# Optimization experiments

Measured on AMD Instinct MI355X. Metric: run time of the kernel, lower is better.

The kernel has to match this reference:

```python
import math
import jax, jax.numpy as jnp
import numpy as np

N_HEAD = 16
ROPE_BASE = 10000.0


def _qk_norm(x, scale):
    # RMSNorm over head_dim, eps added inside sqrt as in the torch code
    norm = jnp.sqrt(jnp.mean(x.astype(jnp.float32) ** 2, axis=-1, keepdims=True) + 1e-6)
    return (x.astype(jnp.float32) / norm * scale).astype(x.dtype)


def _rope3d(q, k, coords, token_type):
    # q,k: [B,H,T,D]; coords: [B,T,3]; token_type: [B,T]
    # head_dim is split into 3 equal chunks, chunk i rotated by coords[...,i].
    # Tokens with token_type == 0 (e.g. text tokens) are left unrotated.
    B, H, T, D = q.shape
    d3 = D // 3
    half = d3 // 2
    inv_freq = ROPE_BASE ** (-jnp.arange(half, dtype=jnp.float32) / half)  # [half]

    def rotate(x):
        # x: [B,H,T,D] -> rotate each of the 3 axis-chunks
        chunks = []
        for a in range(3):
            xa = x[..., a * d3:(a + 1) * d3]                       # [B,H,T,d3]
            ang = coords[:, None, :, a, None] * inv_freq            # [B,1,T,half]
            cos, sin = jnp.cos(ang), jnp.sin(ang)
            x1, x2 = xa[..., :half], xa[..., half:]
            chunks.append(jnp.concatenate([x1 * cos - x2 * sin,
                                           x1 * sin + x2 * cos], axis=-1))
        rot = jnp.concatenate(chunks, axis=-1)
        apply = (token_type > 0)[:, None, :, None]                  # [B,1,T,1]
        return jnp.where(apply, rot, x)

    return rotate(q), rotate(k)


def setup_inputs() -> dict:
    key = jax.random.key(0)
    ks = jax.random.split(key, 5)
    B, T, C = 2, 2048, 1536
    D = C // N_HEAD
    return {
        "x": jax.random.normal(ks[0], (B, T, C), jnp.float32),
        "coords": jax.random.uniform(ks[1], (B, T, 3), jnp.float32) * 32.0,
        "token_type": jax.random.randint(ks[2], (B, T), 0, 2),
        "W_qkv": jax.random.normal(ks[3], (3 * C, C), jnp.float32) * (1.0 / math.sqrt(C)),
        "W_out": jax.random.normal(ks[4], (C, C), jnp.float32) * (1.0 / math.sqrt(C)),
        "q_scale": jnp.ones((D,), jnp.float32),
        "k_scale": jnp.ones((D,), jnp.float32),
    }


def reference(x, coords, token_type, W_qkv, W_out, q_scale, k_scale):
    B, T, C = x.shape
    H = N_HEAD
    D = C // H
    qkv = x @ W_qkv.T                                   # [B,T,3C]
    q, k, v = jnp.split(qkv, 3, axis=-1)
    q = q.reshape(B, T, H, D).transpose(0, 2, 1, 3)     # [B,H,T,D]
    k = k.reshape(B, T, H, D).transpose(0, 2, 1, 3)
    v = v.reshape(B, T, H, D).transpose(0, 2, 1, 3)
    q = _qk_norm(q, q_scale)
    k = _qk_norm(k, k_scale)
    q, k = _rope3d(q, k, coords, token_type)
    scale = 1.0 / math.sqrt(D)
    attn = jnp.einsum('bhqd,bhkd->bhqk', q, k) * scale  # [B,H,T,T]
    causal = jnp.tril(jnp.ones((T, T), bool))
    attn = jnp.where(causal, attn, -jnp.inf)
    attn = jax.nn.softmax(attn, axis=-1)
    out = jnp.einsum('bhqk,bhkd->bhqd', attn, v)        # [B,H,T,D]
    out = out.transpose(0, 2, 1, 3).reshape(B, T, C)
    return out @ W_out.T
```

## Files before the change

### kernel.cpp

```cpp
#include <hip/hip_runtime.h>
#include <stdint.h>
#include <stddef.h>


typedef __attribute__((ext_vector_type(8))) __bf16 bf16x8;
typedef __attribute__((ext_vector_type(4))) __bf16 bf16x4;
typedef __attribute__((ext_vector_type(4))) float  f32x4;

#define NB 2
#define NT 2048
#define NC 1536
#define NH 16
#define ND 96
#define NQKV 4608
#define NM 4096

static __device__ __forceinline__ float fexp2(float x) {
#if __has_builtin(__builtin_amdgcn_exp2f)
  return __builtin_amdgcn_exp2f(x);
#else
  return exp2f(x);
#endif
}

static __device__ __forceinline__ void g2lds16(const void* g, void* l) {
  __builtin_amdgcn_global_load_lds(
      (const __attribute__((address_space(1))) void*)g,
      (__attribute__((address_space(3))) void*)l, 16, 0, 0);
}

__global__ __launch_bounds__(256) void cvt3_f32_bf16(
    const float4* __restrict__ sx, bf16x4* __restrict__ dx, int n4x,
    const float4* __restrict__ sw, bf16x4* __restrict__ dw, int n4w,
    const float4* __restrict__ so, bf16x4* __restrict__ do_) {
  int i = blockIdx.x * 256 + threadIdx.x;
  const float4* s;
  bf16x4* d;
  if (i < n4x)            { s = sx + i;               d = dx + i; }
  else if (i < n4x + n4w) { s = sw + (i - n4x);       d = dw + (i - n4x); }
  else                    { s = so + (i - n4x - n4w); d = do_ + (i - n4x - n4w); }
  float4 v = *s;
  bf16x4 o;
  o[0] = (__bf16)v.x; o[1] = (__bf16)v.y;
  o[2] = (__bf16)v.z; o[3] = (__bf16)v.w;
  *d = o;
}

#define BAR1() do { __builtin_amdgcn_s_barrier(); \
                    asm volatile("" ::: "memory"); } while (0)
#define BAR2() do { asm volatile("" ::: "memory"); \
                    __builtin_amdgcn_s_barrier(); } while (0)
#define WAITLGKM() do { asm volatile("s_waitcnt lgkmcnt(0)" ::: "memory"); \
                        __builtin_amdgcn_sched_barrier(0); } while (0)
#define WAITVM6() asm volatile("s_waitcnt vmcnt(6)" ::: "memory")
#define WAITVM5() asm volatile("s_waitcnt vmcnt(5)" ::: "memory")

template <int MH>
static __device__ __forceinline__ void readA2(
    bf16x8 (&aR)[2][2], const char* buf, int aro, int sk0, int sk1) {
#pragma unroll
  for (int i = 0; i < 2; ++i) {
    const char* p = buf + aro + (MH * 2 + i) * 2048;
    aR[i][0] = *(const bf16x8*)(p + sk0);
    aR[i][1] = *(const bf16x8*)(p + sk1);
  }
}
template <int NF0, int NN>
static __device__ __forceinline__ void readBN(
    bf16x8 (&bb)[NN][2], const char* buf, int bro, int sk0, int sk1) {
#pragma unroll
  for (int j = 0; j < NN; ++j) {
    const char* p = buf + bro + (NF0 + j) * 2048;
    bb[j][0] = *(const bf16x8*)(p + sk0);
    bb[j][1] = *(const bf16x8*)(p + sk1);
  }
}
template <int MH, int NF0, int NN>
static __device__ __forceinline__ void quadN(
    f32x4 (&acc)[4][9], const bf16x8 (&aR)[2][2], const bf16x8 (&bb)[NN][2]) {
  __builtin_amdgcn_s_setprio(1);
#pragma unroll
  for (int i = 0; i < 2; ++i)
#pragma unroll
    for (int j = 0; j < NN; ++j)
#pragma unroll
      for (int ks = 0; ks < 2; ++ks)
        acc[MH * 2 + i][NF0 + j] = __builtin_amdgcn_mfma_f32_16x16x32_bf16(
            aR[i][ks], bb[j][ks], acc[MH * 2 + i][NF0 + j], 0, 0, 0);
  __builtin_amdgcn_s_setprio(0);
}

__global__ __launch_bounds__(512, 2) void gemm1_8ph(
    const __bf16* __restrict__ A, const __bf16* __restrict__ Bw,
    __bf16* __restrict__ C, int M, int N, int K) {
  __shared__ __align__(16) char lds[139264];
  char* const A0 = lds;
  char* const A1 = lds + 32768;
  char* const B0 = lds + 65536;
  char* const B1 = lds + 102400;

  const int tid = threadIdx.x;
  const int l   = tid & 63;
  const int w   = tid >> 6;
  const int wm  = w >> 1;
  const int wn  = w & 1;
  const int lm  = l & 15;
  const int lq  = l >> 4;

  const int nnt = 16;
  const int nwg = gridDim.x * gridDim.y;
  const int lid = blockIdx.y * gridDim.x + blockIdx.x;
  const int swz = (lid & 7) * (nwg >> 3) + (lid >> 3);
  const int m0  = (swz / nnt) * 256;
  const int n0  = (swz % nnt) * 288;

  const int aro = (wm * 64 + lm) * 128;
  const int bro = (wn * 144 + lm) * 128;
  const int sk0 = ((lq) ^ (lm & 7)) * 16;
  const int sk1 = ((4 + lq) ^ (lm & 7)) * 16;

  const int ssl = ((l & 7) ^ ((l >> 3) & 7)) * 8;
  auto stageA = [&](int grow0, int k0, char* dst) {
#pragma unroll
    for (int q2 = 0; q2 < 2; ++q2) {
      const int c   = w * 2 + q2;
      const int row = c * 8 + (l >> 3);
      g2lds16(A + (size_t)(grow0 + row) * K + k0 + ssl, dst + c * 1024);
    }
  };
  auto stageB = [&](int grow0, int k0, char* dst) {
#pragma unroll
    for (int q2 = 0; q2 < 2; ++q2) {
      const int c   = w * 2 + q2;
      const int row = c * 8 + (l >> 3);
      g2lds16(Bw + (size_t)(grow0 + row) * K + k0 + ssl, dst + c * 1024);
    }
    if (w < 2) {
      const int c   = 16 + w;
      const int row = c * 8 + (l >> 3);
      g2lds16(Bw + (size_t)(grow0 + row) * K + k0 + ssl, dst + c * 1024);
    }
  };

  f32x4 acc[4][9] = {};
  bf16x8 aL[2][2], aH[2][2], b5[5][2], b4[4][2];

  stageA(m0,       0,  A0);
  stageA(m0 + 128, 0,  A0 + 16384);
  stageB(n0,       0,  B0);
  stageB(n0 + 144, 0,  B0 + 18432);
  stageA(m0,       64, A1);
  stageA(m0 + 128, 64, A1 + 16384);

  const int NIT = K >> 7;
  for (int it = 0; it < NIT; ++it) {
    const int kh  = it * 128 + 64;
    const int knl = it * 128 + 128;
    const int knh = it * 128 + 192;
    stageB(n0, kh, B1);
    WAITVM6();
    BAR1();
    readA2<0>(aL, A0, aro, sk0, sk1);
    readBN<0, 5>(b5, B0, bro, sk0, sk1);
    WAITLGKM();
    quadN<0, 0, 5>(acc, aL, b5);
    BAR2();
    stageB(n0 + 144, kh, B1 + 18432);
    BAR1();
    readA2<1>(aH, A0, aro, sk0, sk1);
    WAITLGKM();
    quadN<1, 0, 5>(acc, aH, b5);
    BAR2();
    stageA(m0, knl, A0);
    BAR1();
    readBN<5, 4>(b4, B0, bro, sk0, sk1);
    WAITLGKM();
    quadN<1, 5, 4>(acc, aH, b4);
    BAR2();
    stageA(m0 + 128, knl, A0 + 16384);
    BAR1();
    quadN<0, 5, 4>(acc, aL, b4);
    BAR2();
    stageB(n0, knl, B0);
    WAITVM6();
    BAR1();
    readA2<0>(aL, A1, aro, sk0, sk1);
    readBN<0, 5>(b5, B1, bro, sk0, sk1);
    WAITLGKM();
    quadN<0, 0, 5>(acc, aL, b5);
    BAR2();
    stageB(n0 + 144, knl, B0 + 18432);
    BAR1();
    readA2<1>(aH, A1, aro, sk0, sk1);
    WAITLGKM();
    quadN<1, 0, 5>(acc, aH, b5);
    BAR2();
    stageA(m0, knh, A1);
    BAR1();
    readBN<5, 4>(b4, B1, bro, sk0, sk1);
    WAITLGKM();
    quadN<1, 5, 4>(acc, aH, b4);
    BAR2();
    stageA(m0 + 128, knh, A1 + 16384);
    BAR1();
    quadN<0, 5, 4>(acc, aL, b4);
    BAR2();
  }

  const int r0 = lq * 4;
#pragma unroll
  for (int mf = 0; mf < 4; ++mf)
#pragma unroll
    for (int nf = 0; nf < 9; ++nf)
#pragma unroll
      for (int r = 0; r < 4; ++r) {
        const size_t row = (size_t)(m0 + wm * 64 + mf * 16 + r0 + r);
        const size_t col = (size_t)(n0 + wn * 144 + nf * 16 + lm);
        C[row * N + col] = (__bf16)acc[mf][nf][r];
      }
}

template <int MH, int NF0, int NN>
static __device__ __forceinline__ void g2quad(
    f32x4 (&acc)[4][3], const bf16x8 (&aR)[2][2], const bf16x8 (&bb)[NN][2]) {
  __builtin_amdgcn_s_setprio(1);
#pragma unroll
  for (int i = 0; i < 2; ++i)
#pragma unroll
    for (int j = 0; j < NN; ++j)
#pragma unroll
      for (int ks = 0; ks < 2; ++ks)
        acc[MH * 2 + i][NF0 + j] = __builtin_amdgcn_mfma_f32_16x16x32_bf16(
            aR[i][ks], bb[j][ks], acc[MH * 2 + i][NF0 + j], 0, 0, 0);
  __builtin_amdgcn_s_setprio(0);
}

__global__ __launch_bounds__(512, 2) void gemm2_8ph(
    const __bf16* __restrict__ A, const __bf16* __restrict__ Bw,
    float* __restrict__ C, int M, int N, int K) {
  __shared__ __align__(16) char lds[81920];
  char* const A0 = lds;
  char* const A1 = lds + 16384;
  char* const B0 = lds + 32768;
  char* const B1 = lds + 57344;

  const int tid = threadIdx.x;
  const int l   = tid & 63;
  const int w   = tid >> 6;
  const int wm  = w >> 2;
  const int wn  = w & 3;
  const int lm  = l & 15;
  const int lq  = l >> 4;

  const int nwg = gridDim.x * gridDim.y;
  const int lid = blockIdx.y * gridDim.x + blockIdx.x;
  const int swz = (lid & 7) * (nwg >> 3) + (lid >> 3);
  const int m0  = (swz / 8) * 128;
  const int n0  = (swz % 8) * 192;

  const int aro = (wm * 64 + lm) * 128;
  const int bro = (wn * 48 + lm) * 128;
  const int sk0 = ((lq) ^ (lm & 7)) * 16;
  const int sk1 = ((4 + lq) ^ (lm & 7)) * 16;

  const int ssl = ((l & 7) ^ ((l >> 3) & 7)) * 8;
  auto stageA = [&](int k0, char* dst) {
#pragma unroll
    for (int q2 = 0; q2 < 2; ++q2) {
      const int c   = w * 2 + q2;
      const int row = c * 8 + (l >> 3);
      g2lds16(A + (size_t)(m0 + row) * K + k0 + ssl, dst + c * 1024);
    }
  };
  auto stageB = [&](int k0, char* dst) {
#pragma unroll
    for (int q2 = 0; q2 < 3; ++q2) {
      const int c   = w * 3 + q2;
      const int row = c * 8 + (l >> 3);
      g2lds16(Bw + (size_t)(n0 + row) * K + k0 + ssl, dst + c * 1024);
    }
  };

  f32x4 acc[4][3] = {};
  bf16x8 aL[2][2], aH[2][2], bL[2][2], bH[1][2];

  stageA(0,  A0);
  stageB(0,  B0);
  stageA(64, A1);

  const int NIT = K >> 7;
  for (int it = 0; it < NIT; ++it) {
    const int kh  = it * 128 + 64;
    const int knl = it * 128 + 128;
    const int knh = it * 128 + 192;
    stageB(kh, B1);
    WAITVM5();
    BAR1();
    readA2<0>(aL, A0, aro, sk0, sk1);
    readBN<0, 2>(bL, B0, bro, sk0, sk1);
    WAITLGKM();
    g2quad<0, 0, 2>(acc, aL, bL);
    BAR2();
    BAR1();
    readA2<1>(aH, A0, aro, sk0, sk1);
    WAITLGKM();
    g2quad<1, 0, 2>(acc, aH, bL);
    BAR2();
    stageA(knl, A0);
    BAR1();
    readBN<2, 1>(bH, B0, bro, sk0, sk1);
    WAITLGKM();
    g2quad<1, 2, 1>(acc, aH, bH);
    BAR2();
    BAR1();
    g2quad<0, 2, 1>(acc, aL, bH);
    BAR2();
    stageB(knl, B0);
    WAITVM5();
    BAR1();
    readA2<0>(aL, A1, aro, sk0, sk1);
    readBN<0, 2>(bL, B1, bro, sk0, sk1);
    WAITLGKM();
    g2quad<0, 0, 2>(acc, aL, bL);
    BAR2();
    BAR1();
    readA2<1>(aH, A1, aro, sk0, sk1);
    WAITLGKM();
    g2quad<1, 0, 2>(acc, aH, bL);
    BAR2();
    stageA(knh, A1);
    BAR1();
    readBN<2, 1>(bH, B1, bro, sk0, sk1);
    WAITLGKM();
    g2quad<1, 2, 1>(acc, aH, bH);
    BAR2();
    BAR1();
    g2quad<0, 2, 1>(acc, aL, bH);
    BAR2();
  }

  const int r0 = lq * 4;
#pragma unroll
  for (int mf = 0; mf < 4; ++mf)
#pragma unroll
    for (int nf = 0; nf < 3; ++nf)
#pragma unroll
      for (int r = 0; r < 4; ++r) {
        const size_t row = (size_t)(m0 + wm * 64 + mf * 16 + r0 + r);
        const size_t col = (size_t)(n0 + wn * 48 + nf * 16 + lm);
        C[row * N + col] = acc[mf][nf][r];
      }
}

static __device__ __forceinline__ float rope_one(float v, float p, int d,
                                                 const float* c3) {
  const int a  = d >> 5;
  const int j  = d & 31;
  const int jj = j & 15;
  const float invf = fexp2((float)jj * -0.8304820237218406f);
  const float ang  = c3[a] * invf;
  float sn, cs;
  __sincosf(ang, &sn, &cs);
  return (j < 16) ? (v * cs - p * sn) : (v * cs + p * sn);
}

__global__ __launch_bounds__(256) void normrope_kernel(
    const __bf16* __restrict__ qkv, const float* __restrict__ coords,
    const int* __restrict__ ttype, const float* __restrict__ qsc,
    const float* __restrict__ ksc, __bf16* __restrict__ qo,
    __bf16* __restrict__ ko) {
  const int l   = threadIdx.x & 63;
  const int w   = threadIdx.x >> 6;
  const int rid = blockIdx.x * 4 + w;
  const int h   = rid & (NH - 1);
  const int bt  = rid >> 4;
  const int t   = bt & (NT - 1);
  const int b   = bt >> 11;
  const __bf16* base = qkv + (size_t)bt * NQKV + h * ND;
  const float*  c3   = coords + (size_t)bt * 3;
  const bool rope    = ttype[bt] > 0;
  const size_t bh    = (size_t)(b * NH + h);

  {
    float x0 = (float)base[l];
    float x1 = (l < 32) ? (float)base[64 + l] : 0.f;
    float ss = x0 * x0 + x1 * x1;
#pragma unroll
    for (int off = 1; off < 64; off <<= 1) ss += __shfl_xor(ss, off, 64);
    const float rn = rsqrtf(ss * (1.f / 96.f) + 1e-6f);
    x0 *= rn * qsc[l];
    if (l < 32) x1 *= rn * qsc[64 + l];
    const float p0 = __shfl_xor(x0, 16, 64);
    const float p1 = __shfl_xor(x1, 16, 64);
    if (rope) {
      x0 = rope_one(x0, p0, l, c3);
      if (l < 32) x1 = rope_one(x1, p1, 64 + l, c3);
    }
    __bf16* dst = qo + (bh * NT + t) * ND;
    dst[l] = (__bf16)x0;
    if (l < 32) dst[64 + l] = (__bf16)x1;
  }
  {
    float x0 = (float)base[NC + l];
    float x1 = (l < 32) ? (float)base[NC + 64 + l] : 0.f;
    float ss = x0 * x0 + x1 * x1;
#pragma unroll
    for (int off = 1; off < 64; off <<= 1) ss += __shfl_xor(ss, off, 64);
    const float rn = rsqrtf(ss * (1.f / 96.f) + 1e-6f);
    x0 *= rn * ksc[l];
    if (l < 32) x1 *= rn * ksc[64 + l];
    const float p0 = __shfl_xor(x0, 16, 64);
    const float p1 = __shfl_xor(x1, 16, 64);
    if (rope) {
      x0 = rope_one(x0, p0, l, c3);
      if (l < 32) x1 = rope_one(x1, p1, 64 + l, c3);
    }
    __bf16* dst = ko + (bh * NT + t) * ND;
    dst[l] = (__bf16)x0;
    if (l < 32) dst[64 + l] = (__bf16)x1;
  }
}

__global__ __launch_bounds__(256) void transpose_v(
    const __bf16* __restrict__ qkv, __bf16* __restrict__ vo) {
  __shared__ __align__(16) __bf16 tile[96][264];
  const int tid = threadIdx.x;
  const int bh  = blockIdx.y;
  const int t0  = blockIdx.x * 256;
  const int b   = bh >> 4, h = bh & 15;
  const __bf16* src =
      qkv + ((size_t)(b * NT + t0 + tid)) * NQKV + 2 * NC + h * ND;
#pragma unroll
  for (int ch = 0; ch < 12; ++ch) {
    bf16x8 v = *(const bf16x8*)(src + ch * 8);
#pragma unroll
    for (int j = 0; j < 8; ++j) tile[ch * 8 + j][tid] = v[j];
  }
  __syncthreads();
#pragma unroll
  for (int k = 0; k < 12; ++k) {
    const int c  = tid + k * 256;
    const int d  = c >> 5;
    const int tc = c & 31;
    bf16x8 v = *(const bf16x8*)(&tile[d][tc * 8]);
    *(bf16x8*)(vo + ((size_t)bh * ND + d) * NT + t0 + tc * 8) = v;
  }
}

static __device__ __forceinline__ void attn_tile64(
    const bf16x8 (&aq)[3], const bf16x8 (&bk)[4][3], int q0r, int n0,
    int lm, int lq, f32x4& lsum, __bf16* pbase ) {
  f32x4 s[4];
#pragma unroll
  for (int nt = 0; nt < 4; ++nt) {
    f32x4 a = {};
#pragma unroll
    for (int c = 0; c < 3; ++c)
      a = __builtin_amdgcn_mfma_f32_16x16x32_bf16(aq[c], bk[nt][c], a, 0, 0, 0);
    s[nt] = a;
  }
  if (n0 + 63 > q0r) {
#pragma unroll
    for (int nt = 0; nt < 4; ++nt)
#pragma unroll
      for (int r = 0; r < 4; ++r)
        if (n0 + nt * 16 + lm > q0r + lq * 4 + r) s[nt][r] = -1e30f;
  }
  const float cl = 0.10206207261596575f * 1.4426950408889634f;
#pragma unroll
  for (int nt = 0; nt < 4; ++nt)
#pragma unroll
    for (int r = 0; r < 4; ++r)
      s[nt][r] = fexp2((s[nt][r] - 96.0f) * cl);
#pragma unroll
  for (int r = 0; r < 4; ++r)
    lsum[r] += (s[0][r] + s[1][r]) + (s[2][r] + s[3][r]);
#pragma unroll
  for (int nt = 0; nt < 4; ++nt)
#pragma unroll
    for (int r = 0; r < 4; ++r)
      pbase[(nt >> 1) * 640 + (lq * 4 + r) * 40 + (nt & 1) * 16 + lm] =
          (__bf16)s[nt][r];
}

__global__ __launch_bounds__(512) void attn_fwd2(
    const __bf16* __restrict__ q, const __bf16* __restrict__ k,
    const __bf16* __restrict__ vt, __bf16* __restrict__ out) {
  __shared__ __align__(16) char KV[2][24576];
  __shared__ __align__(16) __bf16 plds[8][2][2][16][40];
  const int tid = threadIdx.x;
  const int l   = tid & 63;
  const int w   = tid >> 6;

  const int i_  = blockIdx.y * 8 + blockIdx.x;
  const int slot = i_ >> 3;
  const int bh  = (i_ & 7) + 8 * (slot & 3);
  const int qp  = slot >> 2;

  const int lm  = l & 15;
  const int lq  = l >> 4;
  const int q0L = qp * 128 + w * 16;
  const int q0H = (15 - qp) * 128 + w * 16;
  const int nktLw = qp * 2 + (w >> 2) + 1;
  const int nktHw = (15 - qp) * 2 + (w >> 2) + 1;
  const int nkt   = (15 - qp) * 2 + 2;
  const __bf16* qh = q  + (size_t)bh * NT * ND;
  const __bf16* kh = k  + (size_t)bh * NT * ND;
  const __bf16* vh = vt + (size_t)bh * ND * NT;
  __bf16* pbL = &plds[w][0][0][0][0];
  __bf16* pbH = &plds[w][1][0][0][0];

  auto stage = [&](int n0, char* buf) {
#pragma unroll
    for (int q2 = 0; q2 < 3; ++q2) {
      const int g = w * 3 + q2;
      if (g < 12) {
        const int nt = g / 3, c = g - nt * 3;
        g2lds16(kh + (size_t)(n0 + nt * 16 + (l >> 2)) * ND + c * 32 + (l & 3) * 8,
                buf + g * 1024);
      } else {
        const int gv = g - 12;
        const int dt = gv >> 1, hf = gv & 1;
        g2lds16(vh + (size_t)(dt * 16 + (l >> 2)) * NT + n0 + hf * 32 + (l & 3) * 8,
                buf + 12288 + gv * 1024);
      }
    }
  };

  bf16x8 aqL[3], aqH[3];
#pragma unroll
  for (int c = 0; c < 3; ++c) {
    aqL[c] = *(const bf16x8*)(qh + (size_t)(q0L + lm) * ND + c * 32 + lq * 8);
    aqH[c] = *(const bf16x8*)(qh + (size_t)(q0H + lm) * ND + c * 32 + lq * 8);
  }

  f32x4 oL[6] = {}, oH[6] = {};
  f32x4 lsL = {}, lsH = {};
  const int ji = (lm * 4 + lq) * 16;

  stage(0, KV[0]);
  for (int kt = 0; kt < nkt; ++kt) {
    __syncthreads();
    if (kt + 1 < nkt) stage((kt + 1) * 64, KV[(kt + 1) & 1]);
    const char* Kc = KV[kt & 1];
    const char* Vc = KV[kt & 1] + 12288;
    const int n0 = kt * 64;
    bf16x8 bk[4][3];
#pragma unroll
    for (int nt = 0; nt < 4; ++nt)
#pragma unroll
      for (int c = 0; c < 3; ++c)
        bk[nt][c] = *(const bf16x8*)(Kc + (nt * 3 + c) * 1024 + ji);
    const bool doL = kt < nktLw;
    const bool doH = kt < nktHw;
    if (doL) attn_tile64(aqL, bk, q0L, n0, lm, lq, lsL, pbL);
    if (doH) attn_tile64(aqH, bk, q0H, n0, lm, lq, lsH, pbH);
    bf16x8 apL0 = {}, apL1 = {}, apH0 = {}, apH1 = {};
    if (doL) {
      apL0 = *(const bf16x8*)(pbL + lm * 40 + lq * 8);
      apL1 = *(const bf16x8*)(pbL + 640 + lm * 40 + lq * 8);
    }
    if (doH) {
      apH0 = *(const bf16x8*)(pbH + lm * 40 + lq * 8);
      apH1 = *(const bf16x8*)(pbH + 640 + lm * 40 + lq * 8);
    }
#pragma unroll
    for (int dt = 0; dt < 6; ++dt) {
      bf16x8 bv0 = *(const bf16x8*)(Vc + (dt * 2 + 0) * 1024 + ji);
      bf16x8 bv1 = *(const bf16x8*)(Vc + (dt * 2 + 1) * 1024 + ji);
      if (doL) {
        oL[dt] = __builtin_amdgcn_mfma_f32_16x16x32_bf16(apL0, bv0, oL[dt], 0, 0, 0);
        oL[dt] = __builtin_amdgcn_mfma_f32_16x16x32_bf16(apL1, bv1, oL[dt], 0, 0, 0);
      }
      if (doH) {
        oH[dt] = __builtin_amdgcn_mfma_f32_16x16x32_bf16(apH0, bv0, oH[dt], 0, 0, 0);
        oH[dt] = __builtin_amdgcn_mfma_f32_16x16x32_bf16(apH1, bv1, oH[dt], 0, 0, 0);
      }
    }
  }

  const int b = bh >> 4, h = bh & 15;
#pragma unroll
  for (int f = 0; f < 2; ++f) {
    const f32x4* o = f ? oH : oL;
    const f32x4& ls = f ? lsH : lsL;
    const int q0 = f ? q0H : q0L;
    float rl[4];
#pragma unroll
    for (int r = 0; r < 4; ++r) {
      float v = ls[r];
#pragma unroll
      for (int off = 1; off < 16; off <<= 1) v += __shfl_xor(v, off, 64);
      rl[r] = 1.f / v;
    }
#pragma unroll
    for (int dt = 0; dt < 6; ++dt)
#pragma unroll
      for (int r = 0; r < 4; ++r) {
        const int t = q0 + lq * 4 + r;
        out[((size_t)(b * NT + t)) * NC + h * ND + dt * 16 + lm] =
            (__bf16)(o[dt][r] * rl[r]);
      }
  }
}

static constexpr size_t OFF_XB   = 0;
static constexpr size_t OFF_WQKV = 12582912;
static constexpr size_t OFF_WOUT = 26738688;
static constexpr size_t OFF_QKV  = 31457280;
static constexpr size_t OFF_Q    = 69206016;
static constexpr size_t OFF_K    = 81788928;
static constexpr size_t OFF_VT   = 94371840;

extern "C" void kernel_launch(void* const* d_in, const int* in_sizes, int n_in,
                              void* d_out, int out_size, void* d_ws,
                              size_t ws_size, hipStream_t stream) {
  const float* x      = (const float*)d_in[0];
  const float* coords = (const float*)d_in[1];
  const int*   ttype  = (const int*)d_in[2];
  const float* wqkv   = (const float*)d_in[3];
  const float* wout   = (const float*)d_in[4];
  const float* qs     = (const float*)d_in[5];
  const float* ks     = (const float*)d_in[6];

  char* ws = (char*)d_ws;
  __bf16* xb    = (__bf16*)(ws + OFF_XB);
  __bf16* wqkvb = (__bf16*)(ws + OFF_WQKV);
  __bf16* woutb = (__bf16*)(ws + OFF_WOUT);
  __bf16* qkvb  = (__bf16*)(ws + OFF_QKV);
  __bf16* qb    = (__bf16*)(ws + OFF_Q);
  __bf16* kb    = (__bf16*)(ws + OFF_K);
  __bf16* vtb   = (__bf16*)(ws + OFF_VT);
  __bf16* attnb = (__bf16*)(ws + OFF_XB);

  {
    const int n4x = NM * NC / 4;
    const int n4w = NQKV * NC / 4;
    const int n4o = NC * NC / 4;
    const int nblk = (n4x + n4w + n4o) / 256;
    cvt3_f32_bf16<<<nblk, 256, 0, stream>>>(
        (const float4*)x, (bf16x4*)xb, n4x,
        (const float4*)wqkv, (bf16x4*)wqkvb, n4w,
        (const float4*)wout, (bf16x4*)woutb);
  }
  gemm1_8ph<<<dim3(NQKV / 288, NM / 256), 512, 0, stream>>>(
      xb, wqkvb, qkvb, NM, NQKV, NC);
  normrope_kernel<<<(NB * NT * NH) / 4, 256, 0, stream>>>(
      qkvb, coords, ttype, qs, ks, qb, kb);
  transpose_v<<<dim3(NT / 256, NB * NH), 256, 0, stream>>>(qkvb, vtb);
  attn_fwd2<<<dim3(8, NB * NH), 512, 0, stream>>>(qb, kb, vtb, attnb);
  gemm2_8ph<<<dim3(NC / 192, NM / 128), 512, 0, stream>>>(
      attnb, woutb, (float*)d_out, NM, NC, NC);
}
```

Baseline: 286.7 us.

## Fuse QK RMSNorm, 3D RoPE and V transpose into QKV GEMM epilogue

The QKV projection GEMM now stages its output tile in LDS and applies the per-head RMSNorm and 3D RoPE to Q and K, and transposes V, writing the attention-ready layouts directly. This removes the separate normrope and transpose kernels, two launches, and the write and re-read of the full bf16 QKV intermediate. In exchange the GEMM epilogue becomes serial and heavier, because each head row is handled by a single thread and some threads sit idle. The launch bound no longer requests two blocks per CU, which may lower occupancy.

```diff
diff --git a/kernel.cpp b/kernel.cpp
--- a/kernel.cpp
+++ b/kernel.cpp
@@ -90,9 +90,12 @@
   __builtin_amdgcn_s_setprio(0);
 }
 
-__global__ __launch_bounds__(512, 2) void gemm1_8ph(
+__global__ __launch_bounds__(512) void gemm1_8ph(
     const __bf16* __restrict__ A, const __bf16* __restrict__ Bw,
-    __bf16* __restrict__ C, int M, int N, int K) {
+    const float* __restrict__ coords, const int* __restrict__ ttype,
+    const float* __restrict__ qsc, const float* __restrict__ ksc,
+    __bf16* __restrict__ qo, __bf16* __restrict__ ko,
+    __bf16* __restrict__ vo, int M, int N, int K) {
   __shared__ __align__(16) char lds[139264];
   char* const A0 = lds;
   char* const A1 = lds + 32768;
@@ -207,17 +210,124 @@
     BAR2();
   }
 
-  const int r0 = lq * 4;
-#pragma unroll
-  for (int mf = 0; mf < 4; ++mf)
-#pragma unroll
-    for (int nf = 0; nf < 9; ++nf)
-#pragma unroll
-      for (int r = 0; r < 4; ++r) {
-        const size_t row = (size_t)(m0 + wm * 64 + mf * 16 + r0 + r);
-        const size_t col = (size_t)(n0 + wn * 144 + nf * 16 + lm);
-        C[row * N + col] = (__bf16)acc[mf][nf][r];
+  asm volatile("s_waitcnt vmcnt(0)" ::: "memory");
+  __syncthreads();
+  constexpr int S = 296;
+  __bf16* cl = (__bf16*)lds;
+  const int bI = m0 >> 11;
+  const float IF[16] = {
+      1.0f, 0.5623413251903491f, 0.31622776601683794f, 0.17782794100389226f,
+      0.1f, 0.05623413251903491f, 0.03162277660168379f,
+      0.017782794100389229f, 0.01f, 0.005623413251903491f,
+      0.0031622776601683794f, 0.0017782794100389228f, 0.001f,
+      0.0005623413251903491f, 0.00031622776601683794f,
+      0.00017782794100389227f};
+  for (int half = 0; half < 2; ++half) {
+    if ((wm >> 1) == half) {
+#pragma unroll
+      for (int mf = 0; mf < 4; ++mf)
+#pragma unroll
+        for (int nf = 0; nf < 9; ++nf)
+#pragma unroll
+          for (int r = 0; r < 4; ++r)
+            cl[((wm & 1) * 64 + mf * 16 + lq * 4 + r) * S + wn * 144 +
+               nf * 16 + lm] = (__bf16)acc[mf][nf][r];
+    }
+    __syncthreads();
+    const int rbase = m0 + half * 128;
+    const int tb    = rbase & 2047;
+    const int nact  = half ? 512 : 256;
+    if (tid < nact) {
+      for (int tk = tid; tk < 384; tk += nact) {
+        const int j    = tk >> 7;
+        const int rowl = tk & 127;
+        const int g    = n0 / 96 + j;
+        const int ty   = g >> 4;
+        if (ty < 2) {
+          const int hh   = g & 15;
+          const int rowg = rbase + rowl;
+          const float* c3 = coords + (size_t)rowg * 3;
+          const bool rp   = ttype[rowg] > 0;
+          const float* sc = ty ? ksc : qsc;
+          const __bf16* lr = cl + rowl * S + j * 96;
+          float ss = 0.f;
+#pragma unroll
+          for (int c8 = 0; c8 < 12; ++c8) {
+            bf16x8 v = *(const bf16x8*)(lr + c8 * 8);
+#pragma unroll
+            for (int e = 0; e < 8; ++e) {
+              const float f = (float)v[e];
+              ss += f * f;
+            }
+          }
+          const float rn = rsqrtf(ss * (1.f / 96.f) + 1e-6f);
+          __bf16* dst = (ty ? ko : qo) +
+              ((size_t)((bI * 16 + hh) * 2048 + (rowg & 2047))) * 96;
+#pragma unroll
+          for (int a = 0; a < 3; ++a) {
+            const float ca = c3[a];
+            float xl[16], xh[16];
+            bf16x8 v0 = *(const bf16x8*)(lr + a * 32);
+            bf16x8 v1 = *(const bf16x8*)(lr + a * 32 + 8);
+            bf16x8 v2 = *(const bf16x8*)(lr + a * 32 + 16);
+            bf16x8 v3 = *(const bf16x8*)(lr + a * 32 + 24);
+#pragma unroll
+            for (int e = 0; e < 8; ++e) {
+              xl[e]     = (float)v0[e] * rn * sc[a * 32 + e];
+              xl[e + 8] = (float)v1[e] * rn * sc[a * 32 + 8 + e];
+              xh[e]     = (float)v2[e] * rn * sc[a * 32 + 16 + e];
+              xh[e + 8] = (float)v3[e] * rn * sc[a * 32 + 24 + e];
+            }
+            if (rp) {
+#pragma unroll
+              for (int e = 0; e < 16; ++e) {
+                float sn, csn;
+                __sincosf(ca * IF[e], &sn, &csn);
+                const float lo = xl[e] * csn - xh[e] * sn;
+                const float hi = xl[e] * sn + xh[e] * csn;
+                xl[e] = lo;
+                xh[e] = hi;
+              }
+            }
+            bf16x8 o0, o1, o2, o3;
+#pragma unroll
+            for (int e = 0; e < 8; ++e) {
+              o0[e] = (__bf16)xl[e];
+              o1[e] = (__bf16)xl[e + 8];
+              o2[e] = (__bf16)xh[e];
+              o3[e] = (__bf16)xh[e + 8];
+            }
+            *(bf16x8*)(dst + a * 32)      = o0;
+            *(bf16x8*)(dst + a * 32 + 8)  = o1;
+            *(bf16x8*)(dst + a * 32 + 16) = o2;
+            *(bf16x8*)(dst + a * 32 + 24) = o3;
+          }
+        }
       }
+#pragma unroll
+      for (int j = 0; j < 3; ++j) {
+        const int g = n0 / 96 + j;
+        if (g >= 32) {
+          const int hh = g & 15;
+          for (int tk = tid; tk < 192; tk += nact) {
+            const int d  = tk >> 1;
+            const int sg = tk & 1;
+            const __bf16* cp = cl + (sg * 64) * S + j * 96 + d;
+            __bf16* vdst = vo +
+                ((size_t)(bI * 16 + hh) * 96 + d) * 2048 + tb + sg * 64;
+#pragma unroll
+            for (int vv = 0; vv < 8; ++vv) {
+              bf16x8 ov;
+#pragma unroll
+              for (int e = 0; e < 8; ++e) ov[e] = cp[(vv * 8 + e) * S];
+              *(bf16x8*)(vdst + vv * 8) = ov;
+            }
+          }
+        }
+      }
+    }
+    __syncthreads();
+  }
 }
 
 template <int MH, int NF0, int NN>
@@ -350,101 +460,6 @@
         const size_t col = (size_t)(n0 + wn * 48 + nf * 16 + lm);
         C[row * N + col] = acc[mf][nf][r];
       }
-}
-
-static __device__ __forceinline__ float rope_one(float v, float p, int d,
-                                                 const float* c3) {
-  const int a  = d >> 5;
-  const int j  = d & 31;
-  const int jj = j & 15;
-  const float invf = fexp2((float)jj * -0.8304820237218406f);
-  const float ang  = c3[a] * invf;
-  float sn, cs;
-  __sincosf(ang, &sn, &cs);
-  return (j < 16) ? (v * cs - p * sn) : (v * cs + p * sn);
-}
-
-__global__ __launch_bounds__(256) void normrope_kernel(
-    const __bf16* __restrict__ qkv, const float* __restrict__ coords,
-    const int* __restrict__ ttype, const float* __restrict__ qsc,
-    const float* __restrict__ ksc, __bf16* __restrict__ qo,
-    __bf16* __restrict__ ko) {
-  const int l   = threadIdx.x & 63;
-  const int w   = threadIdx.x >> 6;
-  const int rid = blockIdx.x * 4 + w;
-  const int h   = rid & (NH - 1);
-  const int bt  = rid >> 4;
-  const int t   = bt & (NT - 1);
-  const int b   = bt >> 11;
-  const __bf16* base = qkv + (size_t)bt * NQKV + h * ND;
-  const float*  c3   = coords + (size_t)bt * 3;
-  const bool rope    = ttype[bt] > 0;
-  const size_t bh    = (size_t)(b * NH + h);
-
-  {
-    float x0 = (float)base[l];
-    float x1 = (l < 32) ? (float)base[64 + l] : 0.f;
-    float ss = x0 * x0 + x1 * x1;
-#pragma unroll
-    for (int off = 1; off < 64; off <<= 1) ss += __shfl_xor(ss, off, 64);
-    const float rn = rsqrtf(ss * (1.f / 96.f) + 1e-6f);
-    x0 *= rn * qsc[l];
-    if (l < 32) x1 *= rn * qsc[64 + l];
-    const float p0 = __shfl_xor(x0, 16, 64);
-    const float p1 = __shfl_xor(x1, 16, 64);
-    if (rope) {
-      x0 = rope_one(x0, p0, l, c3);
-      if (l < 32) x1 = rope_one(x1, p1, 64 + l, c3);
-    }
-    __bf16* dst = qo + (bh * NT + t) * ND;
-    dst[l] = (__bf16)x0;
-    if (l < 32) dst[64 + l] = (__bf16)x1;
-  }
-  {
-    float x0 = (float)base[NC + l];
-    float x1 = (l < 32) ? (float)base[NC + 64 + l] : 0.f;
-    float ss = x0 * x0 + x1 * x1;
-#pragma unroll
-    for (int off = 1; off < 64; off <<= 1) ss += __shfl_xor(ss, off, 64);
-    const float rn = rsqrtf(ss * (1.f / 96.f) + 1e-6f);
-    x0 *= rn * ksc[l];
-    if (l < 32) x1 *= rn * ksc[64 + l];
-    const float p0 = __shfl_xor(x0, 16, 64);
-    const float p1 = __shfl_xor(x1, 16, 64);
-    if (rope) {
-      x0 = rope_one(x0, p0, l, c3);
-      if (l < 32) x1 = rope_one(x1, p1, 64 + l, c3);
-    }
-    __bf16* dst = ko + (bh * NT + t) * ND;
-    dst[l] = (__bf16)x0;
-    if (l < 32) dst[64 + l] = (__bf16)x1;
-  }
-}
-
-__global__ __launch_bounds__(256) void transpose_v(
-    const __bf16* __restrict__ qkv, __bf16* __restrict__ vo) {
-  __shared__ __align__(16) __bf16 tile[96][264];
-  const int tid = threadIdx.x;
-  const int bh  = blockIdx.y;
-  const int t0  = blockIdx.x * 256;
-  const int b   = bh >> 4, h = bh & 15;
-  const __bf16* src =
-      qkv + ((size_t)(b * NT + t0 + tid)) * NQKV + 2 * NC + h * ND;
-#pragma unroll
-  for (int ch = 0; ch < 12; ++ch) {
-    bf16x8 v = *(const bf16x8*)(src + ch * 8);
-#pragma unroll
-    for (int j = 0; j < 8; ++j) tile[ch * 8 + j][tid] = v[j];
-  }
-  __syncthreads();
-#pragma unroll
-  for (int k = 0; k < 12; ++k) {
-    const int c  = tid + k * 256;
-    const int d  = c >> 5;
-    const int tc = c & 31;
-    bf16x8 v = *(const bf16x8*)(&tile[d][tc * 8]);
-    *(bf16x8*)(vo + ((size_t)bh * ND + d) * NT + t0 + tc * 8) = v;
-  }
 }
 
 static __device__ __forceinline__ void attn_tile64(
@@ -627,7 +642,6 @@
   __bf16* xb    = (__bf16*)(ws + OFF_XB);
   __bf16* wqkvb = (__bf16*)(ws + OFF_WQKV);
   __bf16* woutb = (__bf16*)(ws + OFF_WOUT);
-  __bf16* qkvb  = (__bf16*)(ws + OFF_QKV);
   __bf16* qb    = (__bf16*)(ws + OFF_Q);
   __bf16* kb    = (__bf16*)(ws + OFF_K);
   __bf16* vtb   = (__bf16*)(ws + OFF_VT);
@@ -644,10 +658,7 @@
         (const float4*)wout, (bf16x4*)woutb);
   }
   gemm1_8ph<<<dim3(NQKV / 288, NM / 256), 512, 0, stream>>>(
-      xb, wqkvb, qkvb, NM, NQKV, NC);
-  normrope_kernel<<<(NB * NT * NH) / 4, 256, 0, stream>>>(
-      qkvb, coords, ttype, qs, ks, qb, kb);
-  transpose_v<<<dim3(NT / 256, NB * NH), 256, 0, stream>>>(qkvb, vtb);
+      xb, wqkvb, coords, ttype, qs, ks, qb, kb, vtb, NM, NQKV, NC);
   attn_fwd2<<<dim3(8, NB * NH), 512, 0, stream>>>(qb, kb, vtb, attnb);
   gemm2_8ph<<<dim3(NC / 192, NM / 128), 512, 0, stream>>>(
       attnb, woutb, (float*)d_out, NM, NC, NC);
```

Result: faster. 263.8 us (-8.0%).
